# Kernel tuning notes

Measured on AMD Instinct MI355X. Metric: run time of the kernel, lower is better.

The kernel has to match this reference:

```python
import jax, jax.numpy as jnp
import numpy as np
from jax import lax

B, S = 4, 2048
HIDDEN = 1024
OUT = 1024
NUM_TABLE = 64
CODE_LEN = 10
TABLE_SIZE = 2 ** CODE_LEN  # 1024
TOTAL_DIM = NUM_TABLE * CODE_LEN  # 640


def setup_inputs() -> dict:
    key = jax.random.key(0)
    k1, k2, k3, k4, k5 = jax.random.split(key, 5)
    hidden_states = jax.random.normal(k1, (B, S, HIDDEN), dtype=jnp.float32)
    # nn.Linear(hidden_size, total_dim): weight [total_dim, hidden] in torch; store as [hidden, total_dim]
    W_proj = jax.random.normal(k2, (HIDDEN, TOTAL_DIM), dtype=jnp.float32) * (1.0 / np.sqrt(HIDDEN))
    b_proj = jax.random.normal(k3, (TOTAL_DIM,), dtype=jnp.float32) * 0.01
    tables = 0.02 * jax.random.normal(k4, (NUM_TABLE * TABLE_SIZE, OUT), dtype=jnp.float32)
    bias = 0.001 * jax.random.normal(k5, (OUT,), dtype=jnp.float32)
    return {"hidden_states": hidden_states, "W_proj": W_proj, "b_proj": b_proj,
            "tables": tables, "bias": bias}


def reference(hidden_states, W_proj, b_proj, tables, bias):
    other_shape = hidden_states.shape[:-1]
    x = hidden_states.reshape(-1, HIDDEN)  # [N, H], N = B*S
    # Hashing: dense projection then per-table code/score
    z = x @ W_proj + b_proj                       # [N, total_dim]
    z = z.reshape(-1, NUM_TABLE, CODE_LEN)        # [N, T, L]
    t = jnp.tanh(jnp.abs(z))
    score = jnp.prod((1.0 + t) * 0.5, axis=-1)    # [N, T] prob of selected bucket
    pow2 = (2 ** jnp.arange(CODE_LEN, dtype=jnp.int32))
    code = jnp.sum((z > 0).astype(jnp.int32) * pow2, axis=-1)  # [N, T] in [0, TABLE_SIZE)

    # Gather + weighted sum over tables, streamed with scan to avoid [N, T, OUT]
    tabs = tables.reshape(NUM_TABLE, TABLE_SIZE, OUT)
    code_t = code.T    # [T, N]
    score_t = score.T  # [T, N]

    def body(acc, inp):
        tab, idx, w = inp  # tab [TABLE_SIZE, OUT], idx [N], w [N]
        return acc + tab[idx] * w[:, None], None

    acc0 = jnp.zeros((x.shape[0], OUT), dtype=hidden_states.dtype)
    out, _ = lax.scan(body, acc0, (tabs, code_t, score_t))
    out = out + bias
    return out.reshape(*other_shape, OUT)
```

## Files before the change

### kernel.cpp

```cpp
#include <hip/hip_runtime.h>
#include <cstddef>
#include <cstdint>

#define HIDDEN    1024
#define OUTD      1024
#define NUM_TABLE 64
#define CODE_LEN  10
#define TABLE_SZ  1024
#define TOTAL_DIM 640

#define TAU   1e-3f
#define FCAP  131072u

typedef float  fx4    __attribute__((ext_vector_type(4)));
typedef ushort ux4    __attribute__((ext_vector_type(4)));
typedef ushort ux8    __attribute__((ext_vector_type(8)));
typedef short  bf16x8 __attribute__((ext_vector_type(8)));
typedef float  f32x4  __attribute__((ext_vector_type(4)));

struct bfp { ushort hi, lo; };
static __device__ __forceinline__ bfp split2(float v) {
    uint32_t u  = __float_as_uint(v);
    float    fh = __uint_as_float(u & 0xFFFF0000u);
    uint32_t ul = __float_as_uint(v - fh);
    bfp r; r.hi = (ushort)(u >> 16); r.lo = (ushort)(ul >> 16);
    return r;
}
static __device__ __forceinline__ ushort f2bf(float f) {
    uint32_t u = __float_as_uint(f);
    return (ushort)((u + 0x7FFFu + ((u >> 16) & 1u)) >> 16);
}

__global__ __launch_bounds__(256)
void split_wt(const float* __restrict__ W, ushort* __restrict__ wht,
              ushort* __restrict__ wlt, float* __restrict__ wt32)
{
    __shared__ float t[32][33];
    const int d0 = blockIdx.x * 32, k0 = blockIdx.y * 32;
    const int lx = threadIdx.x & 31, ly = threadIdx.x >> 5;
    #pragma unroll
    for (int i = 0; i < 32; i += 8)
        t[ly + i][lx] = W[(size_t)(k0 + ly + i) * TOTAL_DIM + d0 + lx];
    __syncthreads();
    #pragma unroll
    for (int i = 0; i < 32; i += 8) {
        float v = t[lx][ly + i];
        bfp s = split2(v);
        size_t o = (size_t)(d0 + ly + i) * HIDDEN + k0 + lx;
        wht[o] = s.hi; wlt[o] = s.lo; wt32[o] = v;
    }
}

#define GBM 64
#define GBN 64
#define GBK 32
#define LDK 40
#define GEMM_MB (8192 / GBM)
#define GEMM_NB (TOTAL_DIM / GBN)
#define GEMM_BLKS (GEMM_MB * GEMM_NB)
#define CONV_BLKS 1024
#define CPG 32
#define NGRP (OUTD / CPG)

__global__ __launch_bounds__(256)
void gemm_convert(const float* __restrict__ x, const ushort* __restrict__ wht,
                  const ushort* __restrict__ wlt, const float* __restrict__ bproj,
                  float* __restrict__ z,
                  const float* __restrict__ tables, ushort* __restrict__ btab)
{
    __shared__ ushort Ah[GBM][LDK];
    __shared__ ushort Al[GBM][LDK];
    __shared__ ushort Bh[GBN][LDK];
    __shared__ ushort Bl[GBN][LDK];

    const int gb  = blockIdx.x;
    const int tid = threadIdx.x;

    if (gb >= GEMM_BLKS) {
        const int cb = gb - GEMM_BLKS;
        const int n4 = NUM_TABLE * TABLE_SZ * (OUTD / 4);
        const fx4* tp = (const fx4*)tables;
        const int stride = CONV_BLKS * 256;
        for (int i = cb * 256 + tid; i < n4; i += stride) {
            fx4 v = __builtin_nontemporal_load(&tp[i]);
            ux4 u;
            u.x = f2bf(v.x); u.y = f2bf(v.y); u.z = f2bf(v.z); u.w = f2bf(v.w);
            int col4 = (i & 255) * 4;
            int row  = (i >> 8) & 1023;
            int t    = i >> 18;
            int g    = col4 >> 5;
            int c    = col4 & 31;
            size_t o = ((((size_t)g * NUM_TABLE + t) * TABLE_SZ + row) << 5) + c;
            *(ux4*)&btab[o] = u;
        }
        return;
    }

    const int lane = tid & 63, wid = tid >> 6;
    const int wr = wid >> 1, wc = wid & 1;
    const int brow = (gb % GEMM_MB) * GBM;
    const int bcol = (gb / GEMM_MB) * GBN;
    const int fr = lane & 15, fq = lane >> 4;

    f32x4 acc[2][2] = {};

    for (int k0 = 0; k0 < HIDDEN; k0 += GBK) {
        #pragma unroll
        for (int i = 0; i < 2; ++i) {
            int c = tid + i * 256;
            int r = c >> 3, kc = (c & 7) * 4;
            fx4 v = *(const fx4*)&x[(size_t)(brow + r) * HIDDEN + k0 + kc];
            bfp s0 = split2(v.x), s1 = split2(v.y), s2 = split2(v.z), s3 = split2(v.w);
            ux4 h, l;
            h.x = s0.hi; l.x = s0.lo;
            h.y = s1.hi; l.y = s1.lo;
            h.z = s2.hi; l.z = s2.lo;
            h.w = s3.hi; l.w = s3.lo;
            *(ux4*)&Ah[r][kc] = h;
            *(ux4*)&Al[r][kc] = l;
        }
        {
            int nr = tid >> 2, kc = (tid & 3) * 8;
            size_t o = (size_t)(bcol + nr) * HIDDEN + k0 + kc;
            *(ux8*)&Bh[nr][kc] = *(const ux8*)&wht[o];
            *(ux8*)&Bl[nr][kc] = *(const ux8*)&wlt[o];
        }
        __syncthreads();

        bf16x8 ah[2], al[2], bh[2], bl[2];
        #pragma unroll
        for (int m = 0; m < 2; ++m) {
            ah[m] = *(const bf16x8*)&Ah[wr * 32 + m * 16 + fr][fq * 8];
            al[m] = *(const bf16x8*)&Al[wr * 32 + m * 16 + fr][fq * 8];
        }
        #pragma unroll
        for (int n = 0; n < 2; ++n) {
            bh[n] = *(const bf16x8*)&Bh[wc * 32 + n * 16 + fr][fq * 8];
            bl[n] = *(const bf16x8*)&Bl[wc * 32 + n * 16 + fr][fq * 8];
        }
        #pragma unroll
        for (int m = 0; m < 2; ++m)
            #pragma unroll
            for (int n = 0; n < 2; ++n) {
                acc[m][n] = __builtin_amdgcn_mfma_f32_16x16x32_bf16(ah[m], bh[n], acc[m][n], 0, 0, 0);
                acc[m][n] = __builtin_amdgcn_mfma_f32_16x16x32_bf16(ah[m], bl[n], acc[m][n], 0, 0, 0);
                acc[m][n] = __builtin_amdgcn_mfma_f32_16x16x32_bf16(al[m], bh[n], acc[m][n], 0, 0, 0);
            }
        __syncthreads();
    }

    #pragma unroll
    for (int n = 0; n < 2; ++n) {
        int col = bcol + wc * 32 + n * 16 + fr;
        float bb = bproj[col];
        #pragma unroll
        for (int m = 0; m < 2; ++m) {
            int rbase = brow + wr * 32 + m * 16 + fq * 4;
            #pragma unroll
            for (int j = 0; j < 4; ++j)
                z[(size_t)(rbase + j) * TOTAL_DIM + col] = acc[m][n][j] + bb;
        }
    }
}

__global__ __launch_bounds__(256)
void code_score2(const float* __restrict__ z, int* __restrict__ code,
                 float* __restrict__ score, uint32_t* __restrict__ flags,
                 uint32_t* __restrict__ cnt, int NT)
{
    int idx = blockIdx.x * 256 + threadIdx.x;
    bool live = idx < NT;
    int n = idx >> 6;
    int t = idx & 63;
    const int lane = threadIdx.x & 63;
    const float* zp = z + (size_t)n * TOTAL_DIM + t * CODE_LEN;
    float s = 1.0f;
    int   c = 0;
    #pragma unroll
    for (int i = 0; i < CODE_LEN; ++i) {
        float v = live ? zp[i] : 1.0f;
        bool  p = fabsf(v) < TAU;
        unsigned long long mask = __ballot(p);
        if (mask) {
            int nact = __popcll(mask);
            int lead = __ffsll((long long)mask) - 1;
            uint32_t base = 0;
            if (lane == lead) base = atomicAdd(cnt, (uint32_t)nact);
            base = (uint32_t)__shfl((int)base, lead);
            if (p) {
                uint32_t slot = base + (uint32_t)__popcll(mask & ((1ull << lane) - 1ull));
                if (slot < FCAP) {
                    uint32_t nd = (uint32_t)(n * TOTAL_DIM + t * CODE_LEN + i);
                    flags[slot] = nd | (v > 0.0f ? 0x80000000u : 0u);
                }
            }
        }
        s *= 0.5f * (1.0f + tanhf(fabsf(v)));
        c |= (v > 0.0f) ? (1 << i) : 0;
    }
    if (live) {
        code[idx]  = c;
        score[idx] = s;
    }
}

__global__ __launch_bounds__(256)
void fixz(const float* __restrict__ x, const float* __restrict__ wt32,
          const float* __restrict__ bproj, int* __restrict__ code,
          const uint32_t* __restrict__ flags, const uint32_t* __restrict__ cnt)
{
    const int lane = threadIdx.x & 63;
    const int gw   = (blockIdx.x * 256 + threadIdx.x) >> 6;
    const int nw   = (gridDim.x * 256) >> 6;
    uint32_t count = *cnt;
    if (count > FCAP) count = FCAP;

    for (uint32_t f = gw; f < count; f += nw) {
        uint32_t fl = flags[f];
        uint32_t e  = fl & 0x7FFFFFFFu;
        int oldpos  = (int)(fl >> 31);
        int n = e / TOTAL_DIM, d = e % TOTAL_DIM;
        const float* xr = x    + (size_t)n * HIDDEN;
        const float* wr = wt32 + (size_t)d * HIDDEN;
        float p = 0.0f;
        #pragma unroll
        for (int j = 0; j < 16; ++j) {
            int k = lane + j * 64;
            p = fmaf(xr[k], wr[k], p);
        }
        #pragma unroll
        for (int off = 32; off; off >>= 1) p += __shfl_xor(p, off);
        float v = p + bproj[d];
        if (lane == 0) {
            if ((v > 0.0f) != (oldpos != 0)) {
                int t = d / CODE_LEN, i = d % CODE_LEN;
                atomicXor(&code[n * NUM_TABLE + t], 1 << i);
            }
        }
    }
}

#define TPB 64
__global__ __launch_bounds__(256)
void gather_grouped(const ushort* __restrict__ btab, const float* __restrict__ bias,
                    const int* __restrict__ code, const float* __restrict__ score,
                    float* __restrict__ out)
{
    __shared__ int   sc[TPB][NUM_TABLE + 1];
    __shared__ float sw[TPB][NUM_TABLE + 1];

    const int b   = blockIdx.x;
    const int g   = (b & 7) + 8 * (b >> 10);
    const int tch = (b >> 3) & 127;
    const int n0  = tch * TPB;
    const int tid = threadIdx.x;

    for (int i = tid; i < TPB * NUM_TABLE; i += 256) {
        int tok = i >> 6, t = i & 63;
        sc[tok][t] = __builtin_nontemporal_load(&code[(n0 + tok) * NUM_TABLE + t]);
        sw[tok][t] = __builtin_nontemporal_load(&score[(n0 + tok) * NUM_TABLE + t]);
    }
    __syncthreads();

    const int tok = tid >> 2;
    const int sub = tid & 3;
    const ushort* tbase = btab + (size_t)g * NUM_TABLE * TABLE_SZ * CPG;

    float acc[8];
    {
        const float* bp = &bias[g * CPG + sub * 8];
        #pragma unroll
        for (int j = 0; j < 8; ++j) acc[j] = bp[j];
    }

    #pragma unroll 4
    for (int t = 0; t < NUM_TABLE; ++t) {
        int   c = sc[tok][t];
        float w = sw[tok][t];
        const ux8 v = *(const ux8*)&tbase[(((size_t)t * TABLE_SZ + c) << 5) + sub * 8];
        #pragma unroll
        for (int j = 0; j < 8; ++j)
            acc[j] += w * __uint_as_float((uint32_t)v[j] << 16);
    }

    fx4 o0 = {acc[0], acc[1], acc[2], acc[3]};
    fx4 o1 = {acc[4], acc[5], acc[6], acc[7]};
    float* op = &out[(size_t)(n0 + tok) * OUTD + g * CPG + sub * 8];
    __builtin_nontemporal_store(o0, (fx4*)op);
    __builtin_nontemporal_store(o1, (fx4*)(op + 4));
}

#define BM 64
#define BN 64
#define BK 32
__global__ __launch_bounds__(256)
void gemm_proj(const float* __restrict__ x, const float* __restrict__ W,
               const float* __restrict__ bproj, float* __restrict__ z)
{
    __shared__ float As[BK][BM + 4];
    __shared__ float Bs[BK][BN];
    const int tid  = threadIdx.x;
    const int brow = blockIdx.x * BM;
    const int bcol = blockIdx.y * BN;
    const int tr   = tid >> 4;
    const int tc   = tid & 15;
    float acc[4][4] = {};
    for (int k0 = 0; k0 < HIDDEN; k0 += BK) {
        #pragma unroll
        for (int i = 0; i < 2; ++i) {
            int lin = tid + i * 256;
            int r = lin >> 3, c8 = lin & 7;
            float4 a = *(const float4*)&x[(size_t)(brow + r) * HIDDEN + k0 + c8 * 4];
            As[c8 * 4 + 0][r] = a.x; As[c8 * 4 + 1][r] = a.y;
            As[c8 * 4 + 2][r] = a.z; As[c8 * 4 + 3][r] = a.w;
        }
        #pragma unroll
        for (int i = 0; i < 2; ++i) {
            int lin = tid + i * 256;
            int kk = lin >> 4, m4 = lin & 15;
            *(float4*)&Bs[kk][m4 * 4] =
                *(const float4*)&W[(size_t)(k0 + kk) * TOTAL_DIM + bcol + m4 * 4];
        }
        __syncthreads();
        #pragma unroll
        for (int kk = 0; kk < BK; ++kk) {
            float4 a = *(const float4*)&As[kk][tr * 4];
            float4 b = *(const float4*)&Bs[kk][tc * 4];
            acc[0][0] += a.x * b.x; acc[0][1] += a.x * b.y; acc[0][2] += a.x * b.z; acc[0][3] += a.x * b.w;
            acc[1][0] += a.y * b.x; acc[1][1] += a.y * b.y; acc[1][2] += a.y * b.z; acc[1][3] += a.y * b.w;
            acc[2][0] += a.z * b.x; acc[2][1] += a.z * b.y; acc[2][2] += a.z * b.z; acc[2][3] += a.z * b.w;
            acc[3][0] += a.w * b.x; acc[3][1] += a.w * b.y; acc[3][2] += a.w * b.z; acc[3][3] += a.w * b.w;
        }
        __syncthreads();
    }
    float4 bb = *(const float4*)&bproj[bcol + tc * 4];
    #pragma unroll
    for (int i = 0; i < 4; ++i) {
        int r = brow + tr * 4 + i;
        float4 o = {acc[i][0] + bb.x, acc[i][1] + bb.y, acc[i][2] + bb.z, acc[i][3] + bb.w};
        *(float4*)&z[(size_t)r * TOTAL_DIM + bcol + tc * 4] = o;
    }
}

__global__ __launch_bounds__(256)
void code_score(const float* __restrict__ z, int* __restrict__ code,
                float* __restrict__ score, int NT)
{
    int idx = blockIdx.x * 256 + threadIdx.x;
    if (idx >= NT) return;
    int n = idx >> 6, t = idx & 63;
    const float* zp = z + (size_t)n * TOTAL_DIM + t * CODE_LEN;
    float s = 1.0f; int c = 0;
    #pragma unroll
    for (int i = 0; i < CODE_LEN; ++i) {
        float v = zp[i];
        s *= 0.5f * (1.0f + tanhf(fabsf(v)));
        c |= (v > 0.0f) ? (1 << i) : 0;
    }
    code[idx] = c; score[idx] = s;
}

__global__ __launch_bounds__(256)
void gather_sum_f32(const float* __restrict__ tables, const float* __restrict__ bias,
                    const int* __restrict__ code, const float* __restrict__ score,
                    float* __restrict__ out)
{
    __shared__ int   sc[NUM_TABLE];
    __shared__ float sw[NUM_TABLE];
    const int n = blockIdx.x, tid = threadIdx.x;
    if (tid < NUM_TABLE) {
        sc[tid] = code[n * NUM_TABLE + tid];
        sw[tid] = score[n * NUM_TABLE + tid];
    }
    __syncthreads();
    float4 acc = *(const float4*)&bias[tid * 4];
    #pragma unroll 4
    for (int t = 0; t < NUM_TABLE; ++t) {
        const float* row = tables + ((size_t)(t * TABLE_SZ + sc[t])) * OUTD;
        float4 v = *(const float4*)&row[tid * 4];
        float w = sw[t];
        acc.x += v.x * w; acc.y += v.y * w; acc.z += v.z * w; acc.w += v.w * w;
    }
    *(float4*)&out[(size_t)n * OUTD + tid * 4] = acc;
}

extern "C" void kernel_launch(void* const* d_in, const int* in_sizes, int n_in,
                              void* d_out, int out_size, void* d_ws, size_t ws_size,
                              hipStream_t stream) {
    const float* x      = (const float*)d_in[0];
    const float* W      = (const float*)d_in[1];
    const float* bproj  = (const float*)d_in[2];
    const float* tables = (const float*)d_in[3];
    const float* bias   = (const float*)d_in[4];
    float* out = (float*)d_out;

    const int N = in_sizes[0] / HIDDEN;

    char* ws = (char*)d_ws;
    size_t off_z     = 0;
    size_t off_code  = off_z     + (size_t)N * TOTAL_DIM * sizeof(float);
    size_t off_score = off_code  + (size_t)N * NUM_TABLE * sizeof(int);
    size_t off_wht   = off_score + (size_t)N * NUM_TABLE * sizeof(float);
    size_t off_wlt   = off_wht   + (size_t)TOTAL_DIM * HIDDEN * sizeof(ushort);
    size_t off_wt32  = off_wlt   + (size_t)TOTAL_DIM * HIDDEN * sizeof(ushort);
    size_t off_flags = off_wt32  + (size_t)TOTAL_DIM * HIDDEN * sizeof(float);
    size_t off_cnt   = off_flags + (size_t)FCAP * sizeof(uint32_t);
    size_t off_btab  = (off_cnt + 4 + 255) & ~(size_t)255;
    size_t tab_elems = (size_t)NUM_TABLE * TABLE_SZ * OUTD;
    size_t need      = off_btab + tab_elems * sizeof(ushort);

    float*    z     = (float*)(ws + off_z);
    int*      code  = (int*)(ws + off_code);
    float*    score = (float*)(ws + off_score);
    ushort*   wht   = (ushort*)(ws + off_wht);
    ushort*   wlt   = (ushort*)(ws + off_wlt);
    float*    wt32  = (float*)(ws + off_wt32);
    uint32_t* flags = (uint32_t*)(ws + off_flags);
    uint32_t* cnt   = (uint32_t*)(ws + off_cnt);
    ushort*   btab  = (ushort*)(ws + off_btab);

    int NT = N * NUM_TABLE;

    if (ws_size >= need) {
        dim3 gw(TOTAL_DIM / 32, HIDDEN / 32);
        split_wt<<<gw, 256, 0, stream>>>(W, wht, wlt, wt32);
        (void)hipMemsetAsync(cnt, 0, 4, stream);

        gemm_convert<<<GEMM_BLKS + CONV_BLKS, 256, 0, stream>>>(
            x, wht, wlt, bproj, z, tables, btab);

        code_score2<<<(NT + 255) / 256, 256, 0, stream>>>(z, code, score, flags, cnt, NT);
        fixz<<<512, 256, 0, stream>>>(x, wt32, bproj, code, flags, cnt);

        gather_grouped<<<NGRP * (N / TPB), 256, 0, stream>>>(btab, bias, code, score, out);
    } else {
        dim3 g1(N / BM, TOTAL_DIM / BN);
        gemm_proj<<<g1, 256, 0, stream>>>(x, W, bproj, z);
        code_score<<<(NT + 255) / 256, 256, 0, stream>>>(z, code, score, NT);
        gather_sum_f32<<<N, 256, 0, stream>>>(tables, bias, code, score, out);
    }
}
```

Before: 325.2 us.

## Double GEMM K-tile with XOR-swizzled LDS and make table conversion writes contiguous

The hashing-projection GEMM now loads a 64-wide K slice per iteration instead of 32. It stores the bf16 hi/lo tiles in LDS with an XOR swizzle rather than row padding, and runs two MFMA sub-steps per barrier pair. This halves the number of sync barriers and widens the global loads. The fp32-to-bf16 table conversion loop is re-indexed to iterate in output order, so stores are fully sequential while reads come in 128-byte strided chunks. The trade-off is more LDS per block and a less sequential read pattern on the large table stream.

```diff
diff --git a/kernel.cpp b/kernel.cpp
--- a/kernel.cpp
+++ b/kernel.cpp
@@ -53,8 +53,7 @@
 
 #define GBM 64
 #define GBN 64
-#define GBK 32
-#define LDK 40
+#define GBK 64
 #define GEMM_MB (8192 / GBM)
 #define GEMM_NB (TOTAL_DIM / GBN)
 #define GEMM_BLKS (GEMM_MB * GEMM_NB)
@@ -68,30 +67,29 @@
                   float* __restrict__ z,
                   const float* __restrict__ tables, ushort* __restrict__ btab)
 {
-    __shared__ ushort Ah[GBM][LDK];
-    __shared__ ushort Al[GBM][LDK];
-    __shared__ ushort Bh[GBN][LDK];
-    __shared__ ushort Bl[GBN][LDK];
+    __shared__ ushort Ah[GBM * GBK];
+    __shared__ ushort Al[GBM * GBK];
+    __shared__ ushort Bh[GBN * GBK];
+    __shared__ ushort Bl[GBN * GBK];
 
     const int gb  = blockIdx.x;
     const int tid = threadIdx.x;
 
     if (gb >= GEMM_BLKS) {
         const int cb = gb - GEMM_BLKS;
-        const int n4 = NUM_TABLE * TABLE_SZ * (OUTD / 4);
+        const int nj = NUM_TABLE * TABLE_SZ * (OUTD / 4);
         const fx4* tp = (const fx4*)tables;
         const int stride = CONV_BLKS * 256;
-        for (int i = cb * 256 + tid; i < n4; i += stride) {
-            fx4 v = __builtin_nontemporal_load(&tp[i]);
+        for (int j = cb * 256 + tid; j < nj; j += stride) {
+            int sub = j & 7;
+            int row = (j >> 3) & 1023;
+            int t   = (j >> 13) & 63;
+            int g   = j >> 19;
+            fx4 v = __builtin_nontemporal_load(
+                        &tp[((size_t)t * TABLE_SZ + row) * 256 + g * 8 + sub]);
             ux4 u;
             u.x = f2bf(v.x); u.y = f2bf(v.y); u.z = f2bf(v.z); u.w = f2bf(v.w);
-            int col4 = (i & 255) * 4;
-            int row  = (i >> 8) & 1023;
-            int t    = i >> 18;
-            int g    = col4 >> 5;
-            int c    = col4 & 31;
-            size_t o = ((((size_t)g * NUM_TABLE + t) * TABLE_SZ + row) << 5) + c;
-            *(ux4*)&btab[o] = u;
+            *(ux4*)&btab[(size_t)j * 4] = u;
         }
         return;
     }
@@ -107,45 +105,59 @@
     for (int k0 = 0; k0 < HIDDEN; k0 += GBK) {
         #pragma unroll
         for (int i = 0; i < 2; ++i) {
-            int c = tid + i * 256;
-            int r = c >> 3, kc = (c & 7) * 4;
-            fx4 v = *(const fx4*)&x[(size_t)(brow + r) * HIDDEN + k0 + kc];
-            bfp s0 = split2(v.x), s1 = split2(v.y), s2 = split2(v.z), s3 = split2(v.w);
-            ux4 h, l;
-            h.x = s0.hi; l.x = s0.lo;
-            h.y = s1.hi; l.y = s1.lo;
-            h.z = s2.hi; l.z = s2.lo;
-            h.w = s3.hi; l.w = s3.lo;
-            *(ux4*)&Ah[r][kc] = h;
-            *(ux4*)&Al[r][kc] = l;
-        }
-        {
-            int nr = tid >> 2, kc = (tid & 3) * 8;
-            size_t o = (size_t)(bcol + nr) * HIDDEN + k0 + kc;
-            *(ux8*)&Bh[nr][kc] = *(const ux8*)&wht[o];
-            *(ux8*)&Bl[nr][kc] = *(const ux8*)&wlt[o];
+            int idx = tid + i * 256;
+            int r = idx >> 3, c8 = idx & 7;
+            const float* xp = &x[(size_t)(brow + r) * HIDDEN + k0 + c8 * 8];
+            fx4 v0 = *(const fx4*)xp;
+            fx4 v1 = *(const fx4*)(xp + 4);
+            bfp s0 = split2(v0.x), s1 = split2(v0.y), s2 = split2(v0.z), s3 = split2(v0.w);
+            bfp s4 = split2(v1.x), s5 = split2(v1.y), s6 = split2(v1.z), s7 = split2(v1.w);
+            ux8 h, l;
+            h[0]=s0.hi; h[1]=s1.hi; h[2]=s2.hi; h[3]=s3.hi;
+            h[4]=s4.hi; h[5]=s5.hi; h[6]=s6.hi; h[7]=s7.hi;
+            l[0]=s0.lo; l[1]=s1.lo; l[2]=s2.lo; l[3]=s3.lo;
+            l[4]=s4.lo; l[5]=s5.lo; l[6]=s6.lo; l[7]=s7.lo;
+            int so = r * GBK + (c8 ^ (r & 7)) * 8;
+            *(ux8*)&Ah[so] = h;
+            *(ux8*)&Al[so] = l;
+        }
+        #pragma unroll
+        for (int i = 0; i < 2; ++i) {
+            int idx = tid + i * 256;
+            int nr = idx >> 3, c8 = idx & 7;
+            size_t o = (size_t)(bcol + nr) * HIDDEN + k0 + c8 * 8;
+            int so = nr * GBK + (c8 ^ (nr & 7)) * 8;
+            *(ux8*)&Bh[so] = *(const ux8*)&wht[o];
+            *(ux8*)&Bl[so] = *(const ux8*)&wlt[o];
         }
         __syncthreads();
 
-        bf16x8 ah[2], al[2], bh[2], bl[2];
-        #pragma unroll
-        for (int m = 0; m < 2; ++m) {
-            ah[m] = *(const bf16x8*)&Ah[wr * 32 + m * 16 + fr][fq * 8];
-            al[m] = *(const bf16x8*)&Al[wr * 32 + m * 16 + fr][fq * 8];
-        }
-        #pragma unroll
-        for (int n = 0; n < 2; ++n) {
-            bh[n] = *(const bf16x8*)&Bh[wc * 32 + n * 16 + fr][fq * 8];
-            bl[n] = *(const bf16x8*)&Bl[wc * 32 + n * 16 + fr][fq * 8];
-        }
-        #pragma unroll
-        for (int m = 0; m < 2; ++m)
+        #pragma unroll
+        for (int kk = 0; kk < 2; ++kk) {
+            bf16x8 ah[2], al[2], bh[2], bl[2];
+            #pragma unroll
+            for (int m = 0; m < 2; ++m) {
+                int r = wr * 32 + m * 16 + fr;
+                int so = r * GBK + (((kk << 2) | fq) ^ (r & 7)) * 8;
+                ah[m] = *(const bf16x8*)&Ah[so];
+                al[m] = *(const bf16x8*)&Al[so];
+            }
             #pragma unroll
             for (int n = 0; n < 2; ++n) {
-                acc[m][n] = __builtin_amdgcn_mfma_f32_16x16x32_bf16(ah[m], bh[n], acc[m][n], 0, 0, 0);
-                acc[m][n] = __builtin_amdgcn_mfma_f32_16x16x32_bf16(ah[m], bl[n], acc[m][n], 0, 0, 0);
-                acc[m][n] = __builtin_amdgcn_mfma_f32_16x16x32_bf16(al[m], bh[n], acc[m][n], 0, 0, 0);
+                int r = wc * 32 + n * 16 + fr;
+                int so = r * GBK + (((kk << 2) | fq) ^ (r & 7)) * 8;
+                bh[n] = *(const bf16x8*)&Bh[so];
+                bl[n] = *(const bf16x8*)&Bl[so];
             }
+            #pragma unroll
+            for (int m = 0; m < 2; ++m)
+                #pragma unroll
+                for (int n = 0; n < 2; ++n) {
+                    acc[m][n] = __builtin_amdgcn_mfma_f32_16x16x32_bf16(ah[m], bh[n], acc[m][n], 0, 0, 0);
+                    acc[m][n] = __builtin_amdgcn_mfma_f32_16x16x32_bf16(ah[m], bl[n], acc[m][n], 0, 0, 0);
+                    acc[m][n] = __builtin_amdgcn_mfma_f32_16x16x32_bf16(al[m], bh[n], acc[m][n], 0, 0, 0);
+                }
+        }
         __syncthreads();
     }
 
```

Measured after the change: 306.7 us. 1.06x faster.
